# Performance work log

Measured on AMD Instinct MI355X. Metric: run time of the kernel, lower is better.

The kernel has to match this reference:

```python
import jax, jax.numpy as jnp
import numpy as np

B, L_DEC, V = 8, 256, 32000
L_SRC = 512
V_EXT = 32128


def setup_inputs() -> dict:
    key = jax.random.key(0)
    k1, k2, k3, k4 = jax.random.split(key, 4)
    dist_t = jax.random.uniform(k1, (B, L_DEC, V), dtype=jnp.float32)
    p_gen = jax.random.uniform(k2, (B, L_DEC, 1), dtype=jnp.float32)
    alph_t = jax.random.uniform(k3, (B, L_SRC, L_DEC), dtype=jnp.float32)
    batch_vocab = jnp.zeros((V_EXT,), dtype=jnp.float32)  # only shape[0] is used
    pointer = jax.random.randint(k4, (B, L_SRC), 0, V_EXT, dtype=jnp.int32)
    return {"dist_t": dist_t, "p_gen": p_gen, "alph_t": alph_t,
            "batch_vocab": batch_vocab, "pointer": pointer}


def reference(dist_t, p_gen, alph_t, batch_vocab, pointer):
    v_ext = batch_vocab.shape[0]
    nb, nl, ndim = dist_t.shape
    # p_gen * [vocab ; zeros padding up to extended vocab]
    prob_vocab = p_gen * jnp.pad(dist_t, ((0, 0), (0, 0), (0, v_ext - ndim)))
    # torch builds a dense one-hot [B, L_src, V_ext] and does bmm(alpha^T, one_hot).
    # Mathematically: copyp[b, t, v] = sum_{s : pointer[b,s]==v} alpha[b, s, t]
    # -> scatter-add of attention weights into pointed vocab slots.
    alpha_td = jnp.swapaxes(alph_t, 1, 2)  # [B, L_dec, L_src]

    def scatter_one(a_td, ptr):  # a_td: [L_dec, L_src], ptr: [L_src]
        return jnp.zeros((a_td.shape[0], v_ext), a_td.dtype).at[:, ptr].add(a_td)

    copyp = jax.vmap(scatter_one)(alpha_td, pointer)  # [B, L_dec, V_ext]
    proba = prob_vocab + (1.0 - p_gen) * copyp
    return proba
```

## Files before the change

### kernel.cpp

```cpp
#include <hip/hip_runtime.h>

#define B_     8
#define L_DEC_ 256
#define V_     32000
#define L_SRC_ 512
#define V_EXT_ 32128

#define V4_    (V_ / 4)
#define VE4_   (V_EXT_ / 4)

#define NMAIN_   15
#define TAIL_I0_ (NMAIN_ * 512)
#define TAIL_N_  (VE4_ - TAIL_I0_)
#define TAIL_ND_ (V4_  - TAIL_I0_)

typedef float f32x4 __attribute__((ext_vector_type(4)));

__global__ __launch_bounds__(512, 8) void copynet_fused(
    const float* __restrict__ dist,
    const float* __restrict__ p_gen,
    const float* __restrict__ alph,
    const int*   __restrict__ pointer,
    float* __restrict__ out)
{
    __shared__ int   head[512];
    __shared__ int   nxt[512];
    __shared__ int   key[512];
    __shared__ float sval[512];

    const int row = blockIdx.x;
    const int b   = row >> 8;
    const int t   = row & (L_DEC_ - 1);
    const int tid = threadIdx.x;

    const float pg   = p_gen[row];
    const float coef = 1.0f - pg;

    const int   sIdx = b * L_SRC_ + tid;
    const int   v    = pointer[sIdx];
    const float val  = coef * alph[(size_t)sIdx * L_DEC_ + t];

    head[tid] = -1;
    __syncthreads();
    key[tid]  = v;
    sval[tid] = val;
    const int owner = (v >> 2) & 511;
    nxt[tid] = atomicExch(&head[owner], tid);
    __syncthreads();

    const int myHead = head[tid];
    unsigned mask = 0u;
    for (int e = myHead; e != -1; e = nxt[e])
        mask |= 1u << (key[e] >> 11);

    const f32x4* dist4 = (const f32x4*)(dist + (size_t)row * V_);
    f32x4*       out4  = (f32x4*)(out + (size_t)row * V_EXT_);

#pragma unroll
    for (int k = 0; k < NMAIN_; ++k) {
        const int i = tid + (k << 9);
        f32x4 r = dist4[i] * pg;
        if (mask & (1u << k)) {
            for (int e = myHead; e != -1; e = nxt[e]) {
                const int kv = key[e];
                if ((kv >> 2) == i) {
                    const float a = sval[e];
                    const int   c = kv & 3;
                    r.x += (c == 0) ? a : 0.f;
                    r.y += (c == 1) ? a : 0.f;
                    r.z += (c == 2) ? a : 0.f;
                    r.w += (c == 3) ? a : 0.f;
                }
            }
        }
        out4[i] = r;
    }

    if (tid < TAIL_N_) {
        const int i = TAIL_I0_ + tid;
        f32x4 r = {0.f, 0.f, 0.f, 0.f};
        if (tid < TAIL_ND_)
            r = dist4[i] * pg;
        if (mask & (1u << 15)) {
            for (int e = myHead; e != -1; e = nxt[e]) {
                const int kv = key[e];
                if ((kv >> 2) == i) {
                    const float a = sval[e];
                    const int   c = kv & 3;
                    r.x += (c == 0) ? a : 0.f;
                    r.y += (c == 1) ? a : 0.f;
                    r.z += (c == 2) ? a : 0.f;
                    r.w += (c == 3) ? a : 0.f;
                }
            }
        }
        out4[i] = r;
    }
}

extern "C" void kernel_launch(void* const* d_in, const int* in_sizes, int n_in,
                              void* d_out, int out_size, void* d_ws, size_t ws_size,
                              hipStream_t stream)
{
    const float* dist    = (const float*)d_in[0];
    const float* p_gen   = (const float*)d_in[1];
    const float* alph    = (const float*)d_in[2];
    const int*   pointer = (const int*)d_in[4];
    float* out = (float*)d_out;

    copynet_fused<<<B_ * L_DEC_, 512, 0, stream>>>(dist, p_gen, alph, pointer, out);
}
```

Before: 446.3 us.

## Precompute per-batch CSR pointer buckets in a separate kernel and stream rows

```diff
diff --git a/kernel.cpp b/kernel.cpp
--- a/kernel.cpp
+++ b/kernel.cpp
@@ -14,20 +14,52 @@
 #define TAIL_N_  (VE4_ - TAIL_I0_)
 #define TAIL_ND_ (V4_  - TAIL_I0_)
 
+#define WS_OFFS_INTS_ (B_ * 513)
+#define WS_BYTES_     (WS_OFFS_INTS_ * 4 + B_ * 512 * 4)
+
 typedef float f32x4 __attribute__((ext_vector_type(4)));
 
-__global__ __launch_bounds__(512, 8) void copynet_fused(
-    const float* __restrict__ dist,
-    const float* __restrict__ p_gen,
-    const float* __restrict__ alph,
-    const int*   __restrict__ pointer,
-    float* __restrict__ out)
+__global__ __launch_bounds__(512) void scatter_pack(
+    const int* __restrict__ pointer,
+    int*       __restrict__ offs_g,
+    unsigned*  __restrict__ ent_g)
 {
-    __shared__ int   head[512];
-    __shared__ int   nxt[512];
-    __shared__ int   key[512];
-    __shared__ float sval[512];
+    __shared__ int cnt[512];
+    __shared__ int sc[512];
+    const int b   = blockIdx.x;
+    const int tid = threadIdx.x;
 
+    cnt[tid] = 0;
+    __syncthreads();
+    const int v     = pointer[b * L_SRC_ + tid];
+    const int owner = (v >> 2) & 511;
+    const int slot  = atomicAdd(&cnt[owner], 1);
+    __syncthreads();
+
+    sc[tid] = cnt[tid];
+    __syncthreads();
+    for (int d = 1; d < 512; d <<= 1) {
+        const int x = (tid >= d) ? sc[tid - d] : 0;
+        __syncthreads();
+        sc[tid] += x;
+        __syncthreads();
+    }
+
+    offs_g[b * 513 + tid] = sc[tid] - cnt[tid];
+    if (tid == 511) offs_g[b * 513 + 512] = sc[511];
+
+    const int base = sc[owner] - cnt[owner];
+    ent_g[b * 512 + base + slot] = (unsigned)v | ((unsigned)tid << 16);
+}
+
+__global__ __launch_bounds__(512, 4) void copynet_stream(
+    const float*    __restrict__ dist,
+    const float*    __restrict__ p_gen,
+    const float*    __restrict__ alph,
+    const int*      __restrict__ offs_g,
+    const unsigned* __restrict__ ent_g,
+    float*          __restrict__ out)
+{
     const int row = blockIdx.x;
     const int b   = row >> 8;
     const int t   = row & (L_DEC_ - 1);
@@ -36,22 +68,15 @@
     const float pg   = p_gen[row];
     const float coef = 1.0f - pg;
 
-    const int   sIdx = b * L_SRC_ + tid;
-    const int   v    = pointer[sIdx];
-    const float val  = coef * alph[(size_t)sIdx * L_DEC_ + t];
+    const int off = offs_g[b * 513 + tid];
+    const int end = offs_g[b * 513 + tid + 1];
 
-    head[tid] = -1;
-    __syncthreads();
-    key[tid]  = v;
-    sval[tid] = val;
-    const int owner = (v >> 2) & 511;
-    nxt[tid] = atomicExch(&head[owner], tid);
-    __syncthreads();
+    const unsigned* entB  = ent_g + b * 512;
+    const float*    alphB = alph + ((size_t)b * L_SRC_) * L_DEC_ + t;
 
-    const int myHead = head[tid];
     unsigned mask = 0u;
-    for (int e = myHead; e != -1; e = nxt[e])
-        mask |= 1u << (key[e] >> 11);
+    for (int e = off; e < end; ++e)
+        mask |= 1u << ((entB[e] >> 11) & 15);
 
     const f32x4* dist4 = (const f32x4*)(dist + (size_t)row * V_);
     f32x4*       out4  = (f32x4*)(out + (size_t)row * V_EXT_);
@@ -59,13 +84,14 @@
 #pragma unroll
     for (int k = 0; k < NMAIN_; ++k) {
         const int i = tid + (k << 9);
-        f32x4 r = dist4[i] * pg;
+        f32x4 r = __builtin_nontemporal_load(dist4 + i) * pg;
         if (mask & (1u << k)) {
-            for (int e = myHead; e != -1; e = nxt[e]) {
-                const int kv = key[e];
-                if ((kv >> 2) == i) {
-                    const float a = sval[e];
-                    const int   c = kv & 3;
+            for (int e = off; e < end; ++e) {
+                const unsigned ev = entB[e];
+                const int v = (int)(ev & 0xffffu);
+                if ((v >> 2) == i) {
+                    const float a = coef * alphB[(ev >> 16) * L_DEC_];
+                    const int   c = v & 3;
                     r.x += (c == 0) ? a : 0.f;
                     r.y += (c == 1) ? a : 0.f;
                     r.z += (c == 2) ? a : 0.f;
@@ -80,18 +106,65 @@
         const int i = TAIL_I0_ + tid;
         f32x4 r = {0.f, 0.f, 0.f, 0.f};
         if (tid < TAIL_ND_)
-            r = dist4[i] * pg;
+            r = __builtin_nontemporal_load(dist4 + i) * pg;
         if (mask & (1u << 15)) {
-            for (int e = myHead; e != -1; e = nxt[e]) {
-                const int kv = key[e];
-                if ((kv >> 2) == i) {
-                    const float a = sval[e];
-                    const int   c = kv & 3;
+            for (int e = off; e < end; ++e) {
+                const unsigned ev = entB[e];
+                const int v = (int)(ev & 0xffffu);
+                if ((v >> 2) == i) {
+                    const float a = coef * alphB[(ev >> 16) * L_DEC_];
+                    const int   c = v & 3;
                     r.x += (c == 0) ? a : 0.f;
                     r.y += (c == 1) ? a : 0.f;
                     r.z += (c == 2) ? a : 0.f;
                     r.w += (c == 3) ? a : 0.f;
                 }
+            }
+        }
+        out4[i] = r;
+    }
+}
+
+__global__ __launch_bounds__(512) void copynet_fused_fallback(
+    const float* __restrict__ dist, const float* __restrict__ p_gen,
+    const float* __restrict__ alph, const int* __restrict__ pointer,
+    float* __restrict__ out)
+{
+    __shared__ int   head[512];
+    __shared__ int   nxt[512];
+    __shared__ int   key[512];
+    __shared__ float sval[512];
+
+    const int row = blockIdx.x, b = row >> 8, t = row & (L_DEC_ - 1);
+    const int tid = threadIdx.x;
+    const float pg = p_gen[row], coef = 1.0f - pg;
+
+    const int   sIdx = b * L_SRC_ + tid;
+    const int   v    = pointer[sIdx];
+    const float val  = coef * alph[(size_t)sIdx * L_DEC_ + t];
+
+    head[tid] = -1;
+    __syncthreads();
+    key[tid] = v; sval[tid] = val;
+    nxt[tid] = atomicExch(&head[(v >> 2) & 511], tid);
+    __syncthreads();
+
+    const int myHead = head[tid];
+    const f32x4* dist4 = (const f32x4*)(dist + (size_t)row * V_);
+    f32x4*       out4  = (f32x4*)(out + (size_t)row * V_EXT_);
+
+    for (int i = tid; i < VE4_; i += 512) {
+        f32x4 r = {0.f, 0.f, 0.f, 0.f};
+        if (i < V4_) r = dist4[i] * pg;
+        for (int e = myHead; e != -1; e = nxt[e]) {
+            const int kv = key[e];
+            if ((kv >> 2) == i) {
+                const float a = sval[e];
+                const int   c = kv & 3;
+                r.x += (c == 0) ? a : 0.f;
+                r.y += (c == 1) ? a : 0.f;
+                r.z += (c == 2) ? a : 0.f;
+                r.w += (c == 3) ? a : 0.f;
             }
         }
         out4[i] = r;
@@ -108,5 +181,14 @@
     const int*   pointer = (const int*)d_in[4];
     float* out = (float*)d_out;
 
-    copynet_fused<<<B_ * L_DEC_, 512, 0, stream>>>(dist, p_gen, alph, pointer, out);
+    if (d_ws != nullptr && ws_size >= (size_t)WS_BYTES_) {
+        int*      offs_g = (int*)d_ws;
+        unsigned* ent_g  = (unsigned*)((char*)d_ws + WS_OFFS_INTS_ * 4);
+        scatter_pack<<<B_, 512, 0, stream>>>(pointer, offs_g, ent_g);
+        copynet_stream<<<B_ * L_DEC_, 512, 0, stream>>>(
+            dist, p_gen, alph, offs_g, ent_g, out);
+    } else {
+        copynet_fused_fallback<<<B_ * L_DEC_, 512, 0, stream>>>(
+            dist, p_gen, alph, pointer, out);
+    }
 }
```

Measured after the change: 482.2 us. +8.0%, slower.
